# Optimization experiments

Hardware: AMD Instinct MI355X
Metric: run time of the kernel (lower is better)

## Reference

```python
import jax, jax.numpy as jnp
import numpy as np

SIGMA = 45.0
N, M, D = 4096, 4096, 1024


def setup_inputs() -> dict:
    key = jax.random.key(0)
    k1, k2 = jax.random.split(key)
    inputs = jax.random.normal(k1, (N, D), dtype=jnp.float32)
    samples = jax.random.normal(k2, (M, D), dtype=jnp.float32)
    return {"inputs": inputs, "samples": samples}


def _sq_dists(x, y):
    # ||x_i||^2 + ||y_j||^2 - 2 x_i.y_j  -> [N, M]
    prod = x @ y.T
    xs = jnp.sum(x * x, axis=1)[:, None]
    ys = jnp.sum(y * y, axis=1)[None, :]
    return xs + ys - 2.0 * prod


def reference(inputs, samples):
    n = inputs.shape[0]
    m = samples.shape[0]
    x = inputs.reshape(n, -1)
    y = samples.reshape(m, -1)
    inv_s2 = 1.0 / (SIGMA ** 2)

    k_xx = _sq_dists(x, x)
    k_yy = _sq_dists(y, y)
    k_xy = _sq_dists(x, y)

    # unbiased MMD: exclude diagonal terms of k_xx, k_yy
    exx = jnp.exp(-k_xx * inv_s2)
    eyy = jnp.exp(-k_yy * inv_s2)
    exy = jnp.exp(-k_xy * inv_s2)

    mmd = (jnp.sum(exx) - jnp.sum(jnp.exp(-jnp.diag(k_xx) * inv_s2))) / (n * (n - 1))
    mmd = mmd + (jnp.sum(eyy) - jnp.sum(jnp.exp(-jnp.diag(k_yy) * inv_s2))) / (m * (m - 1))
    mmd = mmd - 2.0 / (n * m) * jnp.sum(exy)
    return mmd
```

## Files before the change

### kernel.cpp

```cpp
#include <hip/hip_runtime.h>
#include <math.h>


typedef _Float16 f16_t;
typedef _Float16 f16x4 __attribute__((ext_vector_type(4)));
typedef _Float16 f16x8 __attribute__((ext_vector_type(8)));
typedef float floatx4 __attribute__((ext_vector_type(4)));

#define NROWS 4096
#define MROWS 4096
#define DDIM  1024
#define BM    256
#define BN    128
#define BK    32
#define NKT   (DDIM / BK)
#define PSTRIDE (4096 * BK)
#define NTR   (NROWS / BM)
#define NTC   (NROWS / BN)
#define XXB   272
#define NBLK  (2 * XXB + NTR * NTC)

__global__ __launch_bounds__(256) void convert_kernel(
    const float* __restrict__ X, const float* __restrict__ Y,
    f16_t* __restrict__ Xp, f16_t* __restrict__ Yp,
    float* __restrict__ nx, float* __restrict__ ny) {
    const int wid  = threadIdx.x >> 6;
    const int lane = threadIdx.x & 63;
    const int row  = blockIdx.x * 4 + wid;
    const float* src;
    f16_t* dstp;
    float* nrm;
    int r;
    if (row < NROWS) {
        r = row;         src = X + (size_t)r * DDIM;
        dstp = Xp;  nrm = nx;
    } else {
        r = row - NROWS; src = Y + (size_t)r * DDIM;
        dstp = Yp;  nrm = ny;
    }
    const float4* s4 = (const float4*)src;
    float s = 0.f;
    #pragma unroll
    for (int c = 0; c < 4; c++) {
        float4 v = s4[c * 64 + lane];
        f16x4 h;
        h[0] = (f16_t)v.x; h[1] = (f16_t)v.y;
        h[2] = (f16_t)v.z; h[3] = (f16_t)v.w;
        *(f16x4*)(dstp + (size_t)(c * 8 + (lane >> 3)) * PSTRIDE
                       + (size_t)r * BK + (lane & 7) * 4) = h;
        float h0 = (float)h[0], h1 = (float)h[1];
        float h2 = (float)h[2], h3 = (float)h[3];
        s += h0 * h0 + h1 * h1 + h2 * h2 + h3 * h3;
    }
    #pragma unroll
    for (int off = 32; off > 0; off >>= 1) s += __shfl_down(s, off);
    if (lane == 0) nrm[r] = s;
}

#define STAGE(tt_) do {                                                        \
    const int slot_ = (tt_) & 3;                                               \
    const size_t kk_ = (size_t)(((tt_) < NKT) ? (tt_) : (NKT - 1)) * PSTRIDE;  \
    __builtin_amdgcn_global_load_lds(                                          \
        (const __attribute__((address_space(1))) void*)(gA + kk_),             \
        (__attribute__((address_space(3))) void*)(&ldsA[slot_][wave * 1024]),  \
        16, 0, 0);                                                             \
    __builtin_amdgcn_global_load_lds(                                          \
        (const __attribute__((address_space(1))) void*)(gA + kk_ + 16 * BK),   \
        (__attribute__((address_space(3))) void*)(&ldsA[slot_][wave * 1024 + 512]), \
        16, 0, 0);                                                             \
    __builtin_amdgcn_global_load_lds(                                          \
        (const __attribute__((address_space(1))) void*)(gB + kk_),             \
        (__attribute__((address_space(3))) void*)(&ldsB[slot_][wave * 512]),   \
        16, 0, 0);                                                             \
  } while (0)

__global__ __launch_bounds__(512, 2) void mmd_mfma(
    const f16_t* __restrict__ Xp, const f16_t* __restrict__ Yp,
    const float* __restrict__ nx, const float* __restrict__ ny,
    double* __restrict__ partials) {
    __shared__ __align__(16) f16_t ldsA[4][BM * BK];
    __shared__ __align__(16) f16_t ldsB[4][BN * BK];
    __shared__ double wred[8];

    const int b = blockIdx.x;
    const f16_t *Abase, *Bbase;
    const float *nAp, *nBp;
    int arow0, brow0;
    double coef;
    if (b < 2 * XXB) {
        int u = (b < XXB) ? b : b - XXB;
        int i = 0;
        while (u >= NTC - 2 * i) { u -= NTC - 2 * i; i++; }
        const int ti = i, tj = 2 * i + u;
        const double w = (tj >= 2 * i + 2) ? 2.0 : 1.0;
        const f16_t* base;
        const float* nb_;
        double denom;
        if (b < XXB) { base = Xp; nb_ = nx; denom = (double)NROWS * (double)(NROWS - 1); }
        else         { base = Yp; nb_ = ny; denom = (double)MROWS * (double)(MROWS - 1); }
        Abase = base; Bbase = base;
        arow0 = ti * BM;  brow0 = tj * BN;
        nAp = nb_ + ti * BM;  nBp = nb_ + tj * BN;
        coef = w / denom;
    } else {
        const int u = b - 2 * XXB;
        const int ti = u >> 5, tj = u & 31;
        Abase = Xp; Bbase = Yp;
        arow0 = ti * BM;  brow0 = tj * BN;
        nAp = nx + ti * BM;  nBp = ny + tj * BN;
        coef = -2.0 / ((double)NROWS * (double)MROWS);
    }

    const int tid  = threadIdx.x;
    const int wave = tid >> 6;
    const int lane = tid & 63;
    const int wm   = wave >> 1;
    const int wn   = wave & 1;
    const int m    = lane & 15;
    const int quad = lane >> 4;
    const int sw8  = (quad ^ ((m >> 1) & 3)) * 8;
    const int aoff = (wm * 64 + m) * BK + sw8;
    const int boff = (wn * 64 + m) * BK + sw8;

    const int lr = lane >> 2;
    const int lc = (lane & 3) ^ ((lane >> 3) & 3);
    const f16_t* gA = Abase + (size_t)(arow0 + wave * 32 + lr) * BK + lc * 8;
    const f16_t* gB = Bbase + (size_t)(brow0 + wave * 16 + lr) * BK + lc * 8;

    floatx4 acc[4][4];
    #pragma unroll
    for (int i = 0; i < 4; i++)
        #pragma unroll
        for (int j = 0; j < 4; j++) acc[i][j] = (floatx4){0.f, 0.f, 0.f, 0.f};

    STAGE(0); STAGE(1); STAGE(2);
    asm volatile("s_waitcnt vmcnt(6)" ::: "memory");
    __builtin_amdgcn_s_barrier();

    for (int t = 0; t < NKT; ++t) {
        const int slot = t & 3;
        f16x8 ah[4], bh[4];
        #pragma unroll
        for (int s = 0; s < 4; s++) {
            ah[s] = *(const f16x8*)&ldsA[slot][aoff + s * 16 * BK];
            bh[s] = *(const f16x8*)&ldsB[slot][boff + s * 16 * BK];
        }
        STAGE(t + 3);
        asm volatile("s_waitcnt vmcnt(6)" ::: "memory");
        __builtin_amdgcn_s_barrier();
        __builtin_amdgcn_s_setprio(1);
        #pragma unroll
        for (int i = 0; i < 4; i++)
            #pragma unroll
            for (int j = 0; j < 4; j++)
                acc[i][j] = __builtin_amdgcn_mfma_f32_16x16x32_f16(ah[i], bh[j], acc[i][j], 0, 0, 0);
        __builtin_amdgcn_s_setprio(0);
        __builtin_amdgcn_s_barrier();
    }

    const float inv_s2 = 1.0f / 2025.0f;
    float nbv[4];
    #pragma unroll
    for (int j = 0; j < 4; j++) nbv[j] = nBp[wn * 64 + j * 16 + m];
    float lsum = 0.f;
    #pragma unroll
    for (int i = 0; i < 4; i++) {
        floatx4 na4 = *(const floatx4*)&nAp[wm * 64 + i * 16 + quad * 4];
        #pragma unroll
        for (int j = 0; j < 4; j++)
            #pragma unroll
            for (int r = 0; r < 4; r++) {
                float arg = (2.f * acc[i][j][r] - na4[r] - nbv[j]) * inv_s2;
                lsum += __expf(arg);
            }
    }

    double d = (double)lsum;
    #pragma unroll
    for (int off = 32; off > 0; off >>= 1) d += __shfl_down(d, off);
    if (lane == 0) wred[wave] = d;
    __syncthreads();
    if (tid == 0) {
        double s = 0.0;
        #pragma unroll
        for (int w = 0; w < 8; w++) s += wred[w];
        partials[b] = s * coef;
    }
}

__global__ __launch_bounds__(256) void final_reduce(const double* __restrict__ partials,
                                                    float* __restrict__ out) {
    __shared__ double red[256];
    int t = threadIdx.x;
    double s = 0.0;
    for (int i = t; i < NBLK; i += 256) s += partials[i];
    red[t] = s;
    __syncthreads();
    for (int off = 128; off > 0; off >>= 1) {
        if (t < off) red[t] += red[t + off];
        __syncthreads();
    }
    if (t == 0) {
        double mmd = red[0] - 1.0 / (double)(NROWS - 1) - 1.0 / (double)(MROWS - 1);
        out[0] = (float)mmd;
    }
}

extern "C" void kernel_launch(void* const* d_in, const int* in_sizes, int n_in,
                              void* d_out, int out_size, void* d_ws, size_t ws_size,
                              hipStream_t stream) {
    const float* X = (const float*)d_in[0];
    const float* Y = (const float*)d_in[1];
    float* out = (float*)d_out;

    char* p = (char*)d_ws;
    double* partials = (double*)p;            p += ((size_t)NBLK * sizeof(double) + 255) & ~255ULL;
    float* nx = (float*)p;                    p += (size_t)NROWS * sizeof(float);
    float* ny = (float*)p;                    p += (size_t)MROWS * sizeof(float);
    f16_t* Xp = (f16_t*)p;                    p += (size_t)NROWS * DDIM * sizeof(f16_t);
    f16_t* Yp = (f16_t*)p;

    convert_kernel<<<(NROWS + MROWS) / 4, 256, 0, stream>>>(X, Y, Xp, Yp, nx, ny);
    mmd_mfma<<<NBLK, 512, 0, stream>>>(Xp, Yp, nx, ny, partials);
    final_reduce<<<1, 256, 0, stream>>>(partials, out);
}
```

Measured before the change: 165.5 us.

## Software-pipeline LDS reads with MFMA using register double buffering

Restructures the K-loop so the LDS fragment reads for the next tile go into a second register set while MFMAs consume the current one. The loop is unrolled by four with explicit prologue and epilogue, and the prefetch depth drops from three tiles to two. There is now one barrier per k-step instead of two, and the out-of-range clamped loads are gone. This trades more VGPRs (two fragment sets) and shallower global prefetch for fewer barriers and better overlap of ds_read with MFMA; the single barrier per step needs careful checking for slot reuse races.

After: 166.6 us. Within noise of the previous version (+0.6%).

```diff
diff --git a/kernel.cpp b/kernel.cpp
--- a/kernel.cpp
+++ b/kernel.cpp
@@ -59,7 +59,7 @@
 
 #define STAGE(tt_) do {                                                        \
     const int slot_ = (tt_) & 3;                                               \
-    const size_t kk_ = (size_t)(((tt_) < NKT) ? (tt_) : (NKT - 1)) * PSTRIDE;  \
+    const size_t kk_ = (size_t)(tt_) * PSTRIDE;                                \
     __builtin_amdgcn_global_load_lds(                                          \
         (const __attribute__((address_space(1))) void*)(gA + kk_),             \
         (__attribute__((address_space(3))) void*)(&ldsA[slot_][wave * 1024]),  \
@@ -72,6 +72,29 @@
         (const __attribute__((address_space(1))) void*)(gB + kk_),             \
         (__attribute__((address_space(3))) void*)(&ldsB[slot_][wave * 512]),   \
         16, 0, 0);                                                             \
+  } while (0)
+
+#define VMCNT3 asm volatile("s_waitcnt vmcnt(3)" ::: "memory")
+#define VMCNT0 asm volatile("s_waitcnt vmcnt(0)" ::: "memory")
+#define BAR    __builtin_amdgcn_s_barrier()
+
+#define DSREAD(slot_, AH_, BH_) do {                                           \
+    _Pragma("unroll")                                                          \
+    for (int s_ = 0; s_ < 4; s_++) {                                           \
+        AH_[s_] = *(const f16x8*)&ldsA[slot_][aoff + s_ * 16 * BK];            \
+        BH_[s_] = *(const f16x8*)&ldsB[slot_][boff + s_ * 16 * BK];            \
+    }                                                                          \
+  } while (0)
+
+#define MFMA16(AH_, BH_) do {                                                  \
+    __builtin_amdgcn_s_setprio(1);                                             \
+    _Pragma("unroll")                                                          \
+    for (int i_ = 0; i_ < 4; i_++)                                             \
+        _Pragma("unroll")                                                      \
+        for (int j_ = 0; j_ < 4; j_++)                                         \
+            acc[i_][j_] = __builtin_amdgcn_mfma_f32_16x16x32_f16(              \
+                AH_[i_], BH_[j_], acc[i_][j_], 0, 0, 0);                       \
+    __builtin_amdgcn_s_setprio(0);                                             \
   } while (0)
 
 __global__ __launch_bounds__(512, 2) void mmd_mfma(
@@ -133,30 +156,23 @@
         #pragma unroll
         for (int j = 0; j < 4; j++) acc[i][j] = (floatx4){0.f, 0.f, 0.f, 0.f};
 
-    STAGE(0); STAGE(1); STAGE(2);
-    asm volatile("s_waitcnt vmcnt(6)" ::: "memory");
-    __builtin_amdgcn_s_barrier();
-
-    for (int t = 0; t < NKT; ++t) {
-        const int slot = t & 3;
-        f16x8 ah[4], bh[4];
-        #pragma unroll
-        for (int s = 0; s < 4; s++) {
-            ah[s] = *(const f16x8*)&ldsA[slot][aoff + s * 16 * BK];
-            bh[s] = *(const f16x8*)&ldsB[slot][boff + s * 16 * BK];
-        }
-        STAGE(t + 3);
-        asm volatile("s_waitcnt vmcnt(6)" ::: "memory");
-        __builtin_amdgcn_s_barrier();
-        __builtin_amdgcn_s_setprio(1);
-        #pragma unroll
-        for (int i = 0; i < 4; i++)
-            #pragma unroll
-            for (int j = 0; j < 4; j++)
-                acc[i][j] = __builtin_amdgcn_mfma_f32_16x16x32_f16(ah[i], bh[j], acc[i][j], 0, 0, 0);
-        __builtin_amdgcn_s_setprio(0);
-        __builtin_amdgcn_s_barrier();
-    }
+    f16x8 ahA[4], bhA[4], ahB[4], bhB[4];
+
+    STAGE(0); STAGE(1);
+    VMCNT3;
+    BAR;
+    DSREAD(0, ahA, bhA);
+
+    for (int tt = 0; tt < NKT - 4; tt += 4) {
+        STAGE(tt + 2); VMCNT3; BAR; DSREAD(1, ahB, bhB); MFMA16(ahA, bhA);
+        STAGE(tt + 3); VMCNT3; BAR; DSREAD(2, ahA, bhA); MFMA16(ahB, bhB);
+        STAGE(tt + 4); VMCNT3; BAR; DSREAD(3, ahB, bhB); MFMA16(ahA, bhA);
+        STAGE(tt + 5); VMCNT3; BAR; DSREAD(0, ahA, bhA); MFMA16(ahB, bhB);
+    }
+    STAGE(30); VMCNT3; BAR; DSREAD(1, ahB, bhB); MFMA16(ahA, bhA);
+    STAGE(31); VMCNT3; BAR; DSREAD(2, ahA, bhA); MFMA16(ahB, bhB);
+    VMCNT0;              BAR; DSREAD(3, ahB, bhB); MFMA16(ahA, bhA);
+    MFMA16(ahB, bhB);
 
     const float inv_s2 = 1.0f / 2025.0f;
     float nbv[4];
```
